# Performance work log

Hardware: AMD Instinct MI355X
Metric: run time of the kernel (lower is better)

## Reference

```python
import jax, jax.numpy as jnp
import numpy as np

TAU = 32.0


def setup_inputs() -> dict:
    key = jax.random.key(0)
    k1, k2, k3, k4, k5 = jax.random.split(key, 5)
    B, IN, E, D, M = 32768, 768, 256, 9, 10
    feature = jax.random.normal(k1, (B, IN), dtype=jnp.float32)
    category = jax.random.randint(k2, (B,), 0, D)  # unused in forward math
    # nn.Linear(input_dim, emb_dim, bias=False) stores weight [emb_dim, input_dim]
    W_topic = jax.random.normal(k3, (E, IN), dtype=jnp.float32) * (1.0 / np.sqrt(IN))
    W_domain = jax.random.normal(k4, (E, IN), dtype=jnp.float32) * (1.0 / np.sqrt(IN))
    memory = jax.random.normal(k5, (D, M, E), dtype=jnp.float32)  # stacked domain memory banks
    return {"feature": feature, "category": category, "W_topic": W_topic,
            "W_domain": W_domain, "memory": memory}


def reference(feature, category, W_topic, W_domain, memory):
    # L2-normalize features along dim 1
    f = feature / jnp.linalg.norm(feature, axis=1, keepdims=True)
    topic = f @ W_topic.T      # [B, E]
    dom = f @ W_domain.T       # [B, E]
    # per-domain memory attention, batched over all D domains at once
    att = jax.nn.softmax(jnp.einsum('be,dme->bdm', topic, memory) * TAU, axis=-1)  # [B, D, M]
    sep = jnp.einsum('bdm,dme->bde', att, memory)                                   # [B, D, E]
    domain_att = jnp.einsum('bde,be->bd', sep, dom)                                 # [B, D]
    return jax.nn.softmax(domain_att * TAU, axis=1)[:, None, :]                     # [B, 1, D]
```

## Files before the change

### kernel.cpp

```cpp
#include <hip/hip_runtime.h>
#include <math.h>

typedef __attribute__((ext_vector_type(8))) short short8;
typedef __attribute__((ext_vector_type(4))) float f32x4;
typedef __attribute__((ext_vector_type(8))) unsigned short u16x8;

#define TAUF 32.0f
#define SB() __builtin_amdgcn_sched_barrier(0)
#define BAR() __builtin_amdgcn_s_barrier()

constexpr int A_SZ     = 16384;
constexpr int B_BASE   = 32768;
constexpr int B_LO_OFF = 12288;
constexpr int B_SZ     = 24576;
constexpr int CSTR     = 196;

__global__ __launch_bounds__(768) void precompute_pr(
    const float* __restrict__ Wt, const float* __restrict__ Wd,
    const float* __restrict__ mem, unsigned short* __restrict__ PRhi,
    unsigned short* __restrict__ PRlo) {
  int r0 = blockIdx.x * 6, t = threadIdx.x;
  if (r0 >= 180) {
    #pragma unroll
    for (int rr = 0; rr < 6; ++rr) {
      PRhi[(size_t)(r0 + rr) * 768 + t] = 0;
      PRlo[(size_t)(r0 + rr) * 768 + t] = 0;
    }
    return;
  }
  __shared__ float mlds[1536];
  const float* W = (r0 >= 90) ? Wd : Wt;
  int dm0 = (r0 >= 90) ? r0 - 90 : r0;
  for (int i = t; i < 1536; i += 768) mlds[i] = mem[(size_t)dm0 * 256 + i];
  __syncthreads();
  float a[6] = {0.f, 0.f, 0.f, 0.f, 0.f, 0.f};
  #pragma unroll 4
  for (int e = 0; e < 256; ++e) {
    float w = W[(size_t)e * 768 + t];
    #pragma unroll
    for (int rr = 0; rr < 6; ++rr) a[rr] += mlds[rr * 256 + e] * w;
  }
  #pragma unroll
  for (int rr = 0; rr < 6; ++rr) {
    unsigned int bu = __float_as_uint(a[rr]);
    unsigned short hi = (unsigned short)(bu >> 16);
    float hf = __uint_as_float(bu & 0xffff0000u);
    unsigned short lo = (unsigned short)(__float_as_uint(a[rr] - hf) >> 16);
    PRhi[(size_t)(r0 + rr) * 768 + t] = hi;
    PRlo[(size_t)(r0 + rr) * 768 + t] = lo;
  }
}

__global__ __launch_bounds__(512) void fused_mfma(
    const float* __restrict__ feat, const unsigned short* __restrict__ PRhi,
    const unsigned short* __restrict__ PRlo, float* __restrict__ out) {
  __shared__ f32x4 smemv[5120];
  __shared__ float invn[128];
  __shared__ float sarr[576];
  char* smem = (char*)smemv;

  const int t    = threadIdx.x;
  const int lane = t & 63;
  const int wid  = t >> 6;
  const int rg   = wid >> 1;
  const int cg   = wid & 1;
  const int b0   = blockIdx.x * 128;

  const char* featB = (const char*)feat;

  auto issueA = [&](int kt, int bb) {
    #pragma unroll
    for (int u = 0; u < 2; ++u) {
      int G   = (wid * 2 + u) * 64 + lane;
      int row = G >> 3;
      int kq  = (G & 7) ^ (row & 7);
      const char* src = featB + (size_t)(b0 + row) * 3072 + kt * 128 + kq * 16;
      char* dst = smem + bb * A_SZ + G * 16;
      __builtin_amdgcn_global_load_lds((const unsigned int*)src,
                                       (unsigned int*)dst, 16, 0, 0);
    }
  };

  const int iid  = wid * 3;
  const int bc   = lane >> 2;
  const int bsw  = (lane & 3) ^ ((bc >> 1) & 3);
  const int bsrc = bc * 1536 + bsw * 16;

  auto issueB = [&](int kt, int bb) {
    #pragma unroll
    for (int u = 0; u < 3; ++u) {
      int i  = iid + u;
      int pl = i >= 12;
      int ch = pl ? i - 12 : i;
      const unsigned short* basep = pl ? PRlo : PRhi;
      const char* gg = (const char*)basep + (size_t)ch * 16 * 1536 +
                       kt * 64 + bsrc;
      char* l = smem + B_BASE + bb * B_SZ + (pl ? B_LO_OFF : 0) + ch * 1024 +
                lane * 16;
      __builtin_amdgcn_global_load_lds((const unsigned int*)gg,
                                       (unsigned int*)l, 16, 0, 0);
    }
  };

  const int bfr = ((lane & 15) << 6) |
                  ((((lane >> 4) ^ (((lane & 15) >> 1) & 3)) & 3) << 4);

  f32x4 acc0[6], acc1[6];
  #pragma unroll
  for (int j = 0; j < 6; ++j) {
    acc0[j] = (f32x4){0.f, 0.f, 0.f, 0.f};
    acc1[j] = (f32x4){0.f, 0.f, 0.f, 0.f};
  }
  float ssq0 = 0.f, ssq1 = 0.f;

  short8 ah0, al0, ah1, al1;

  auto readA = [&](int bb) {
    char* base = smem + bb * A_SZ;
    const int c = lane >> 4;
    #pragma unroll
    for (int rt = 0; rt < 2; ++rt) {
      int row = rg * 32 + rt * 16 + (lane & 15);
      int p0  = (2 * c)     ^ (row & 7);
      int p1  = (2 * c + 1) ^ (row & 7);
      f32x4 v0 = *(const f32x4*)(base + row * 128 + p0 * 16);
      f32x4 v1 = *(const f32x4*)(base + row * 128 + p1 * 16);
      float xs[8] = {v0[0], v0[1], v0[2], v0[3], v1[0], v1[1], v1[2], v1[3]};
      u16x8 h, l;
      float ss = 0.f;
      #pragma unroll
      for (int e = 0; e < 8; ++e) {
        float x = xs[e];
        ss += x * x;
        unsigned int bu = __float_as_uint(x);
        h[e] = (unsigned short)(bu >> 16);
        l[e] = (unsigned short)(__float_as_uint(
                   x - __uint_as_float(bu & 0xffff0000u)) >> 16);
      }
      if (rt == 0) { ah0 = (short8)h; al0 = (short8)l; ssq0 += ss; }
      else         { ah1 = (short8)h; al1 = (short8)l; ssq1 += ss; }
    }
  };

  auto domfma = [&](int bb) {
    char* base = smem + B_BASE + bb * B_SZ;
    #pragma unroll
    for (int j = 0; j < 6; ++j) {
      int chb = (cg * 6 + j) * 1024;
      short8 bh = *(const short8*)(base + chb + bfr);
      short8 bl = *(const short8*)(base + B_LO_OFF + chb + bfr);
      acc0[j] = __builtin_amdgcn_mfma_f32_16x16x32_bf16(ah0, bh, acc0[j], 0, 0, 0);
      acc0[j] = __builtin_amdgcn_mfma_f32_16x16x32_bf16(al0, bh, acc0[j], 0, 0, 0);
      acc0[j] = __builtin_amdgcn_mfma_f32_16x16x32_bf16(ah0, bl, acc0[j], 0, 0, 0);
      acc1[j] = __builtin_amdgcn_mfma_f32_16x16x32_bf16(ah1, bh, acc1[j], 0, 0, 0);
      acc1[j] = __builtin_amdgcn_mfma_f32_16x16x32_bf16(al1, bh, acc1[j], 0, 0, 0);
      acc1[j] = __builtin_amdgcn_mfma_f32_16x16x32_bf16(ah1, bl, acc1[j], 0, 0, 0);
    }
  };

  issueA(0, 0); issueB(0, 0);
  issueA(1, 1); issueB(1, 1);
  asm volatile("s_waitcnt vmcnt(5)" ::: "memory");
  SB(); BAR();

  for (int kp = 0; kp < 11; ++kp) {
    int kt = 2 * kp;
    readA(0);
    domfma(0);
    SB(); BAR();
    issueA(kt + 2, 0); issueB(kt + 2, 0);
    asm volatile("s_waitcnt vmcnt(5)" ::: "memory");
    SB(); BAR();
    readA(1);
    domfma(1);
    SB(); BAR();
    issueA(kt + 3, 1); issueB(kt + 3, 1);
    asm volatile("s_waitcnt vmcnt(5)" ::: "memory");
    SB(); BAR();
  }
  readA(0);
  domfma(0);
  SB(); BAR();
  asm volatile("s_waitcnt vmcnt(0)" ::: "memory");
  SB(); BAR();
  readA(1);
  domfma(1);

  float v0 = ssq0, v1 = ssq1;
  v0 += __shfl_xor(v0, 16, 64); v0 += __shfl_xor(v0, 32, 64);
  v1 += __shfl_xor(v1, 16, 64); v1 += __shfl_xor(v1, 32, 64);
  if (cg == 0 && lane < 16) {
    invn[rg * 32 + lane]      = rsqrtf(v0);
    invn[rg * 32 + 16 + lane] = rsqrtf(v1);
  }
  __syncthreads();

  float* Clds = (float*)smem;
  for (int ph = 0; ph < 2; ++ph) {
    if ((rg >> 1) == ph) {
      int lrow = (rg & 1) * 32;
      #pragma unroll
      for (int rt = 0; rt < 2; ++rt) {
        int rbase = lrow + rt * 16 + ((lane >> 4) << 2);
        int grow  = ph * 64 + rbase;
        #pragma unroll
        for (int j = 0; j < 6; ++j) {
          int col = cg * 96 + j * 16 + (lane & 15);
          f32x4 v = rt ? acc1[j] : acc0[j];
          #pragma unroll
          for (int jj = 0; jj < 4; ++jj)
            Clds[(rbase + jj) * CSTR + col] = v[jj] * invn[grow + jj];
        }
      }
    }
    __syncthreads();

    for (int pid = t; pid < 576; pid += 512) {
      int row = pid / 9, d = pid - row * 9;
      const float* qp = Clds + row * CSTR + d * 10;
      const float* rp = qp + 90;
      float mx = qp[0];
      #pragma unroll
      for (int m = 1; m < 10; ++m) mx = fmaxf(mx, qp[m]);
      float s = 0.f, val = 0.f;
      #pragma unroll
      for (int m = 0; m < 10; ++m) {
        float e = __expf(TAUF * (qp[m] - mx));
        s += e;
        val += e * rp[m];
      }
      sarr[pid] = val / s;
    }
    __syncthreads();

    if (t < 64) {
      float v2[9];
      #pragma unroll
      for (int d = 0; d < 9; ++d) v2[d] = sarr[t * 9 + d];
      float mx = v2[0];
      #pragma unroll
      for (int d = 1; d < 9; ++d) mx = fmaxf(mx, v2[d]);
      float s = 0.f;
      float e[9];
      #pragma unroll
      for (int d = 0; d < 9; ++d) {
        e[d] = __expf(TAUF * (v2[d] - mx));
        s += e[d];
      }
      float is = 1.f / s;
      #pragma unroll
      for (int d = 0; d < 9; ++d)
        out[(size_t)(b0 + ph * 64 + t) * 9 + d] = e[d] * is;
    }
    __syncthreads();
  }
}

extern "C" void kernel_launch(void* const* d_in, const int* in_sizes, int n_in,
                              void* d_out, int out_size, void* d_ws, size_t ws_size,
                              hipStream_t stream) {
  const float* feat = (const float*)d_in[0];
  const float* Wt  = (const float*)d_in[2];
  const float* Wd  = (const float*)d_in[3];
  const float* mem = (const float*)d_in[4];
  float* outp = (float*)d_out;

  unsigned short* PRhi = (unsigned short*)d_ws;
  unsigned short* PRlo = PRhi + 192 * 768;

  precompute_pr<<<32, 768, 0, stream>>>(Wt, Wd, mem, PRhi, PRlo);
  const int B = in_sizes[1];
  fused_mfma<<<B / 128, 512, 0, stream>>>(feat, PRhi, PRlo, outp);
}
```

Measured before the change: 71.07 us.

## Halve block row tile, double K-step per stage, raise MFMA wave priority

The fused kernel now uses 64-row blocks of 256 threads instead of 128-row blocks of 512. Each pipeline stage loads a 64-wide K slice, so there are half as many barrier-separated stages. LDS per block grows to 128KB with two 64KB buffers. The epilogue becomes a single pass, and s_setprio is raised around the MFMA bursts. The aim is fewer barriers and more loads in flight per stage, at the cost of lower occupancy and twice as many blocks each reading the shared projection matrix.

Result: slower. 86.22 us (+21.3%).

```diff
diff --git a/kernel.cpp b/kernel.cpp
--- a/kernel.cpp
+++ b/kernel.cpp
@@ -9,11 +9,9 @@
 #define SB() __builtin_amdgcn_sched_barrier(0)
 #define BAR() __builtin_amdgcn_s_barrier()
 
-constexpr int A_SZ     = 16384;
-constexpr int B_BASE   = 32768;
-constexpr int B_LO_OFF = 12288;
-constexpr int B_SZ     = 24576;
-constexpr int CSTR     = 196;
+constexpr int A_SZ  = 16384;
+constexpr int BUF   = 65536;
+constexpr int CSTR  = 196;
 
 __global__ __launch_bounds__(768) void precompute_pr(
     const float* __restrict__ Wt, const float* __restrict__ Wd,
@@ -51,11 +49,11 @@
   }
 }
 
-__global__ __launch_bounds__(512) void fused_mfma(
+__global__ __launch_bounds__(256) void fused_mfma(
     const float* __restrict__ feat, const unsigned short* __restrict__ PRhi,
     const unsigned short* __restrict__ PRlo, float* __restrict__ out) {
-  __shared__ f32x4 smemv[5120];
-  __shared__ float invn[128];
+  __shared__ f32x4 smemv[8192];
+  __shared__ float invn[64];
   __shared__ float sarr[576];
   char* smem = (char*)smemv;
 
@@ -64,39 +62,40 @@
   const int wid  = t >> 6;
   const int rg   = wid >> 1;
   const int cg   = wid & 1;
-  const int b0   = blockIdx.x * 128;
-
+  const int b0   = blockIdx.x * 64;
   const char* featB = (const char*)feat;
 
   auto issueA = [&](int kt, int bb) {
     #pragma unroll
-    for (int u = 0; u < 2; ++u) {
-      int G   = (wid * 2 + u) * 64 + lane;
-      int row = G >> 3;
-      int kq  = (G & 7) ^ (row & 7);
-      const char* src = featB + (size_t)(b0 + row) * 3072 + kt * 128 + kq * 16;
-      char* dst = smem + bb * A_SZ + G * 16;
+    for (int u = 0; u < 4; ++u) {
+      int G   = (wid * 4 + u) * 64 + lane;
+      int row = G >> 4;
+      int s   = G & 15;
+      int kq  = s ^ (row & 15);
+      const char* src = featB + (size_t)(b0 + row) * 3072 + kt * 256 + kq * 16;
+      char* dst = smem + bb * BUF + G * 16;
       __builtin_amdgcn_global_load_lds((const unsigned int*)src,
                                        (unsigned int*)dst, 16, 0, 0);
     }
   };
 
-  const int iid  = wid * 3;
   const int bc   = lane >> 2;
   const int bsw  = (lane & 3) ^ ((bc >> 1) & 3);
   const int bsrc = bc * 1536 + bsw * 16;
 
   auto issueB = [&](int kt, int bb) {
     #pragma unroll
-    for (int u = 0; u < 3; ++u) {
-      int i  = iid + u;
-      int pl = i >= 12;
-      int ch = pl ? i - 12 : i;
+    for (int u = 0; u < 12; ++u) {
+      int i  = wid * 12 + u;
+      int pl = i >= 24;
+      int j  = pl ? i - 24 : i;
+      int ks = j >= 12;
+      int ch = ks ? j - 12 : j;
       const unsigned short* basep = pl ? PRlo : PRhi;
       const char* gg = (const char*)basep + (size_t)ch * 16 * 1536 +
-                       kt * 64 + bsrc;
-      char* l = smem + B_BASE + bb * B_SZ + (pl ? B_LO_OFF : 0) + ch * 1024 +
-                lane * 16;
+                       kt * 128 + ks * 64 + bsrc;
+      char* l = smem + bb * BUF + A_SZ + ks * 24576 + (pl ? 12288 : 0) +
+                ch * 1024 + lane * 16;
       __builtin_amdgcn_global_load_lds((const unsigned int*)gg,
                                        (unsigned int*)l, 16, 0, 0);
     }
@@ -115,16 +114,17 @@
 
   short8 ah0, al0, ah1, al1;
 
-  auto readA = [&](int bb) {
-    char* base = smem + bb * A_SZ;
+  auto readA = [&](int bb, int ks) {
+    char* base = smem + bb * BUF;
     const int c = lane >> 4;
     #pragma unroll
     for (int rt = 0; rt < 2; ++rt) {
       int row = rg * 32 + rt * 16 + (lane & 15);
-      int p0  = (2 * c)     ^ (row & 7);
-      int p1  = (2 * c + 1) ^ (row & 7);
-      f32x4 v0 = *(const f32x4*)(base + row * 128 + p0 * 16);
-      f32x4 v1 = *(const f32x4*)(base + row * 128 + p1 * 16);
+      int k0  = ks * 8 + 2 * c;
+      int p0  = k0 ^ (row & 15);
+      int p1  = (k0 + 1) ^ (row & 15);
+      f32x4 v0 = *(const f32x4*)(base + row * 256 + p0 * 16);
+      f32x4 v1 = *(const f32x4*)(base + row * 256 + p1 * 16);
       float xs[8] = {v0[0], v0[1], v0[2], v0[3], v1[0], v1[1], v1[2], v1[3]};
       u16x8 h, l;
       float ss = 0.f;
@@ -142,13 +142,14 @@
     }
   };
 
-  auto domfma = [&](int bb) {
-    char* base = smem + B_BASE + bb * B_SZ;
+  auto domfma = [&](int bb, int ks) {
+    char* base = smem + bb * BUF + A_SZ + ks * 24576;
+    __builtin_amdgcn_s_setprio(1);
     #pragma unroll
     for (int j = 0; j < 6; ++j) {
       int chb = (cg * 6 + j) * 1024;
       short8 bh = *(const short8*)(base + chb + bfr);
-      short8 bl = *(const short8*)(base + B_LO_OFF + chb + bfr);
+      short8 bl = *(const short8*)(base + 12288 + chb + bfr);
       acc0[j] = __builtin_amdgcn_mfma_f32_16x16x32_bf16(ah0, bh, acc0[j], 0, 0, 0);
       acc0[j] = __builtin_amdgcn_mfma_f32_16x16x32_bf16(al0, bh, acc0[j], 0, 0, 0);
       acc0[j] = __builtin_amdgcn_mfma_f32_16x16x32_bf16(ah0, bl, acc0[j], 0, 0, 0);
@@ -156,35 +157,39 @@
       acc1[j] = __builtin_amdgcn_mfma_f32_16x16x32_bf16(al1, bh, acc1[j], 0, 0, 0);
       acc1[j] = __builtin_amdgcn_mfma_f32_16x16x32_bf16(ah1, bl, acc1[j], 0, 0, 0);
     }
-  };
+    __builtin_amdgcn_s_setprio(0);
+  };
+
+#define COMPUTE(bb)                                                          \
+  readA(bb, 0);                                                              \
+  domfma(bb, 0);                                                             \
+  readA(bb, 1);                                                              \
+  domfma(bb, 1);
 
   issueA(0, 0); issueB(0, 0);
   issueA(1, 1); issueB(1, 1);
-  asm volatile("s_waitcnt vmcnt(5)" ::: "memory");
+  asm volatile("s_waitcnt vmcnt(16)" ::: "memory");
   SB(); BAR();
 
-  for (int kp = 0; kp < 11; ++kp) {
+  for (int kp = 0; kp < 5; ++kp) {
     int kt = 2 * kp;
-    readA(0);
-    domfma(0);
+    COMPUTE(0)
     SB(); BAR();
     issueA(kt + 2, 0); issueB(kt + 2, 0);
-    asm volatile("s_waitcnt vmcnt(5)" ::: "memory");
-    SB(); BAR();
-    readA(1);
-    domfma(1);
+    asm volatile("s_waitcnt vmcnt(16)" ::: "memory");
+    SB(); BAR();
+    COMPUTE(1)
     SB(); BAR();
     issueA(kt + 3, 1); issueB(kt + 3, 1);
-    asm volatile("s_waitcnt vmcnt(5)" ::: "memory");
-    SB(); BAR();
-  }
-  readA(0);
-  domfma(0);
+    asm volatile("s_waitcnt vmcnt(16)" ::: "memory");
+    SB(); BAR();
+  }
+  COMPUTE(0)
   SB(); BAR();
   asm volatile("s_waitcnt vmcnt(0)" ::: "memory");
   SB(); BAR();
-  readA(1);
-  domfma(1);
+  COMPUTE(1)
+#undef COMPUTE
 
   float v0 = ssq0, v1 = ssq1;
   v0 += __shfl_xor(v0, 16, 64); v0 += __shfl_xor(v0, 32, 64);
@@ -196,63 +201,56 @@
   __syncthreads();
 
   float* Clds = (float*)smem;
-  for (int ph = 0; ph < 2; ++ph) {
-    if ((rg >> 1) == ph) {
-      int lrow = (rg & 1) * 32;
+  #pragma unroll
+  for (int rt = 0; rt < 2; ++rt) {
+    int rbase = rg * 32 + rt * 16 + ((lane >> 4) << 2);
+    #pragma unroll
+    for (int j = 0; j < 6; ++j) {
+      int col = cg * 96 + j * 16 + (lane & 15);
+      f32x4 v = rt ? acc1[j] : acc0[j];
       #pragma unroll
-      for (int rt = 0; rt < 2; ++rt) {
-        int rbase = lrow + rt * 16 + ((lane >> 4) << 2);
-        int grow  = ph * 64 + rbase;
-        #pragma unroll
-        for (int j = 0; j < 6; ++j) {
-          int col = cg * 96 + j * 16 + (lane & 15);
-          f32x4 v = rt ? acc1[j] : acc0[j];
-          #pragma unroll
-          for (int jj = 0; jj < 4; ++jj)
-            Clds[(rbase + jj) * CSTR + col] = v[jj] * invn[grow + jj];
-        }
-      }
-    }
-    __syncthreads();
-
-    for (int pid = t; pid < 576; pid += 512) {
-      int row = pid / 9, d = pid - row * 9;
-      const float* qp = Clds + row * CSTR + d * 10;
-      const float* rp = qp + 90;
-      float mx = qp[0];
-      #pragma unroll
-      for (int m = 1; m < 10; ++m) mx = fmaxf(mx, qp[m]);
-      float s = 0.f, val = 0.f;
-      #pragma unroll
-      for (int m = 0; m < 10; ++m) {
-        float e = __expf(TAUF * (qp[m] - mx));
-        s += e;
-        val += e * rp[m];
-      }
-      sarr[pid] = val / s;
-    }
-    __syncthreads();
-
-    if (t < 64) {
-      float v2[9];
-      #pragma unroll
-      for (int d = 0; d < 9; ++d) v2[d] = sarr[t * 9 + d];
-      float mx = v2[0];
-      #pragma unroll
-      for (int d = 1; d < 9; ++d) mx = fmaxf(mx, v2[d]);
-      float s = 0.f;
-      float e[9];
-      #pragma unroll
-      for (int d = 0; d < 9; ++d) {
-        e[d] = __expf(TAUF * (v2[d] - mx));
-        s += e[d];
-      }
-      float is = 1.f / s;
-      #pragma unroll
-      for (int d = 0; d < 9; ++d)
-        out[(size_t)(b0 + ph * 64 + t) * 9 + d] = e[d] * is;
-    }
-    __syncthreads();
+      for (int jj = 0; jj < 4; ++jj)
+        Clds[(rbase + jj) * CSTR + col] = v[jj] * invn[rbase + jj];
+    }
+  }
+  __syncthreads();
+
+  for (int pid = t; pid < 576; pid += 256) {
+    int row = pid / 9, d = pid - row * 9;
+    const float* qp = Clds + row * CSTR + d * 10;
+    const float* rp = qp + 90;
+    float mx = qp[0];
+    #pragma unroll
+    for (int m = 1; m < 10; ++m) mx = fmaxf(mx, qp[m]);
+    float s = 0.f, val = 0.f;
+    #pragma unroll
+    for (int m = 0; m < 10; ++m) {
+      float e = __expf(TAUF * (qp[m] - mx));
+      s += e;
+      val += e * rp[m];
+    }
+    sarr[pid] = val / s;
+  }
+  __syncthreads();
+
+  if (t < 64) {
+    float v2[9];
+    #pragma unroll
+    for (int d = 0; d < 9; ++d) v2[d] = sarr[t * 9 + d];
+    float mx = v2[0];
+    #pragma unroll
+    for (int d = 1; d < 9; ++d) mx = fmaxf(mx, v2[d]);
+    float s = 0.f;
+    float e[9];
+    #pragma unroll
+    for (int d = 0; d < 9; ++d) {
+      e[d] = __expf(TAUF * (v2[d] - mx));
+      s += e[d];
+    }
+    float is = 1.f / s;
+    #pragma unroll
+    for (int d = 0; d < 9; ++d)
+      out[(size_t)(b0 + t) * 9 + d] = e[d] * is;
   }
 }
 
@@ -270,5 +268,5 @@
 
   precompute_pr<<<32, 768, 0, stream>>>(Wt, Wd, mem, PRhi, PRlo);
   const int B = in_sizes[1];
-  fused_mfma<<<B / 128, 512, 0, stream>>>(feat, PRhi, PRlo, outp);
+  fused_mfma<<<B / 64, 256, 0, stream>>>(feat, PRhi, PRlo, outp);
 }
```
